# Performance work log

Measured on AMD Instinct MI355X. Metric: run time of the kernel, lower is better.

Reference implementation:

```python
import jax, jax.numpy as jnp
import numpy as np

N_RULES = 64  # R
OUT_PER_RULE = 64  # O, fc out = R*O = 4096


def setup_inputs() -> dict:
    key = jax.random.key(0)
    k1, k2, k3, k4 = jax.random.split(key, 4)
    S, D_IN = 8192, 1024
    RO = N_RULES * OUT_PER_RULE
    X = jax.random.normal(k1, (S, D_IN), dtype=jnp.float32)
    # torch.nn.Linear-style weight [out, in] and bias [out]
    W = jax.random.normal(k2, (RO, D_IN), dtype=jnp.float32) * (1.0 / np.sqrt(D_IN))
    b = jax.random.normal(k3, (RO,), dtype=jnp.float32) * 0.01
    # rule firing strengths (computed under no_grad in the original)
    lambdas = jax.random.uniform(k4, (S, N_RULES), dtype=jnp.float32)
    return {"X": X, "W": W, "b": b, "lambdas": lambdas}


def reference(X, W, b, lambdas):
    # fc + sigmoid: [S, R*O]
    H = jax.nn.sigmoid(X @ W.T + b)
    S = H.shape[0]
    # apply_rule_strength: block-diagonal lambda_eye @ H^T is exactly a
    # rule-weighted sum over the R consecutive O-sized blocks of H.
    Hr = H.reshape(S, N_RULES, OUT_PER_RULE)  # [S, R, O]
    Y = jnp.einsum("sr,sro->so", lambdas, Hr)  # [S, O]
    return Y
```

## Files before the change

kernel.cpp:

```cpp
#include <hip/hip_runtime.h>

#define S_DIM 8192
#define K_DIM 1024
#define RO_DIM 4096
#define O_DIM 64
#define SO (S_DIM * O_DIM)

typedef __attribute__((ext_vector_type(8))) __bf16 bf16x8;
typedef __attribute__((ext_vector_type(4))) float floatx4;
typedef __attribute__((ext_vector_type(4))) unsigned short ushx4;

__device__ inline unsigned short f2bf(float f) {
  unsigned u = __builtin_bit_cast(unsigned, f);
  u += 0x7fff + ((u >> 16) & 1);
  return (unsigned short)(u >> 16);
}
__device__ inline float bf2f(unsigned short h) {
  unsigned u = ((unsigned)h) << 16;
  return __builtin_bit_cast(float, u);
}

__global__ __launch_bounds__(256) void cast_kernel(const float* __restrict__ X,
                                                   const float* __restrict__ W,
                                                   unsigned short* __restrict__ Xb,
                                                   unsigned short* __restrict__ Wb) {
  int i = blockIdx.x * 256 + threadIdx.x;
  const int NX4 = (S_DIM * K_DIM) / 4;
  float4 v;
  unsigned short* dst;
  if (i < NX4) {
    v = ((const float4*)X)[i];
    dst = Xb + (size_t)i * 4;
  } else {
    int j = i - NX4;
    v = ((const float4*)W)[j];
    dst = Wb + (size_t)j * 4;
  }
  ushx4 o;
  o.x = f2bf(v.x); o.y = f2bf(v.y); o.z = f2bf(v.z); o.w = f2bf(v.w);
  *(ushx4*)dst = o;
}

__global__ __launch_bounds__(256) void gemm_kernel(const unsigned short* __restrict__ Xb,
                                                   const unsigned short* __restrict__ Wb,
                                                   const float* __restrict__ bias,
                                                   const float* __restrict__ lam,
                                                   unsigned short* __restrict__ partial) {
  __shared__ __align__(16) unsigned char smem[32768];
  unsigned short* Atile = (unsigned short*)smem;
  unsigned short* Btile = (unsigned short*)(smem + 8192);
  float* ypart = (float*)smem;

  const int t = threadIdx.x;
  const int lane = t & 63;
  const int w = t >> 6;
  const int wm = w & 1;
  const int wn = w >> 1;
  const int quad = lane >> 4;
  const int l16 = lane & 15;
  const int gm0 = blockIdx.y * 128;
  const int gn0 = blockIdx.x * 128;

  floatx4 acc[4][4];
#pragma unroll
  for (int mi = 0; mi < 4; ++mi)
#pragma unroll
    for (int ni = 0; ni < 4; ++ni) acc[mi][ni] = (floatx4){0.f, 0.f, 0.f, 0.f};

  for (int k0 = 0; k0 < K_DIM; k0 += 32) {
    __syncthreads();
#pragma unroll
    for (int i = 0; i < 2; ++i) {
      int idx = i * 256 + t;
      int row = idx >> 2;
      int cc = idx & 3;
      int gcc = cc ^ ((row >> 1) & 3);
      const unsigned short* ga = Xb + (size_t)(gm0 + row) * K_DIM + k0 + gcc * 8;
      const unsigned short* gb = Wb + (size_t)(gn0 + row) * K_DIM + k0 + gcc * 8;
      __builtin_amdgcn_global_load_lds(
          (const __attribute__((address_space(1))) void*)ga,
          (__attribute__((address_space(3))) void*)(Atile + idx * 8), 16, 0, 0);
      __builtin_amdgcn_global_load_lds(
          (const __attribute__((address_space(1))) void*)gb,
          (__attribute__((address_space(3))) void*)(Btile + idx * 8), 16, 0, 0);
    }
    __syncthreads();

    bf16x8 af[4], bfr[4];
#pragma unroll
    for (int mi = 0; mi < 4; ++mi) {
      int row = wm * 64 + mi * 16 + l16;
      int cc = quad ^ ((row >> 1) & 3);
      af[mi] = *(const bf16x8*)(Atile + row * 32 + cc * 8);
    }
#pragma unroll
    for (int ni = 0; ni < 4; ++ni) {
      int row = wn * 64 + ni * 16 + l16;
      int cc = quad ^ ((row >> 1) & 3);
      bfr[ni] = *(const bf16x8*)(Btile + row * 32 + cc * 8);
    }
#pragma unroll
    for (int mi = 0; mi < 4; ++mi)
#pragma unroll
      for (int ni = 0; ni < 4; ++ni)
        acc[mi][ni] = __builtin_amdgcn_mfma_f32_16x16x32_bf16(af[mi], bfr[ni], acc[mi][ni], 0, 0, 0);
  }

  const int rule = blockIdx.x * 2 + wn;
  float bv[4];
#pragma unroll
  for (int ni = 0; ni < 4; ++ni) bv[ni] = bias[gn0 + wn * 64 + ni * 16 + l16];

  __syncthreads();
  if (wn == 0) {
#pragma unroll
    for (int mi = 0; mi < 4; ++mi) {
#pragma unroll
      for (int reg = 0; reg < 4; ++reg) {
        int row = wm * 64 + mi * 16 + quad * 4 + reg;
        float lv = lam[(size_t)(gm0 + row) * 64 + rule];
#pragma unroll
        for (int ni = 0; ni < 4; ++ni) {
          float z = acc[mi][ni][reg] + bv[ni];
          float h = 1.f / (1.f + __expf(-z));
          ypart[row * O_DIM + ni * 16 + l16] = lv * h;
        }
      }
    }
  }
  __syncthreads();
  if (wn == 1) {
#pragma unroll
    for (int mi = 0; mi < 4; ++mi) {
#pragma unroll
      for (int reg = 0; reg < 4; ++reg) {
        int row = wm * 64 + mi * 16 + quad * 4 + reg;
        float lv = lam[(size_t)(gm0 + row) * 64 + rule];
#pragma unroll
        for (int ni = 0; ni < 4; ++ni) {
          float z = acc[mi][ni][reg] + bv[ni];
          float h = 1.f / (1.f + __expf(-z));
          ypart[row * O_DIM + ni * 16 + l16] += lv * h;
        }
      }
    }
  }
  __syncthreads();

  unsigned short* pdst = partial + (size_t)blockIdx.x * SO + (size_t)gm0 * O_DIM;
#pragma unroll
  for (int j = 0; j < 8; ++j) {
    int q = j * 256 + t;
    const float* src = ypart + q * 4;
    ushx4 o;
    o.x = f2bf(src[0]); o.y = f2bf(src[1]); o.z = f2bf(src[2]); o.w = f2bf(src[3]);
    ((ushx4*)pdst)[q] = o;
  }
}

__global__ __launch_bounds__(256) void reduce_kernel(const unsigned short* __restrict__ partial,
                                                     float* __restrict__ Y) {
  int i4 = blockIdx.x * 256 + threadIdx.x;
  float s0 = 0.f, s1 = 0.f, s2 = 0.f, s3 = 0.f;
#pragma unroll
  for (int c = 0; c < 32; ++c) {
    ushx4 v = ((const ushx4*)(partial + (size_t)c * SO))[i4];
    s0 += bf2f(v.x); s1 += bf2f(v.y); s2 += bf2f(v.z); s3 += bf2f(v.w);
  }
  ((float4*)Y)[i4] = (float4){s0, s1, s2, s3};
}

extern "C" void kernel_launch(void* const* d_in, const int* in_sizes, int n_in,
                              void* d_out, int out_size, void* d_ws, size_t ws_size,
                              hipStream_t stream) {
  const float* X = (const float*)d_in[0];
  const float* W = (const float*)d_in[1];
  const float* b = (const float*)d_in[2];
  const float* lam = (const float*)d_in[3];
  float* Y = (float*)d_out;

  unsigned short* Xb = (unsigned short*)d_ws;
  unsigned short* Wb = Xb + (size_t)S_DIM * K_DIM;
  unsigned short* partial = Wb + (size_t)RO_DIM * K_DIM;

  int nCast = ((S_DIM + RO_DIM) * K_DIM / 4) / 256;
  cast_kernel<<<nCast, 256, 0, stream>>>(X, W, Xb, Wb);

  dim3 g(RO_DIM / 128, S_DIM / 128);
  gemm_kernel<<<g, 256, 0, stream>>>(Xb, Wb, b, lam, partial);

  reduce_kernel<<<SO / 1024, 256, 0, stream>>>(partial, Y);
}
```

Before: 206.6 us.

## Switch GEMM to 32x32x16 MFMA and fuse rule reduction via LDS atomics

Replaces the 4x4 grid of 16x16x32 bf16 MFMA tiles per wave with a 2x2 grid of 32x32x16 tiles, split into two k-substeps per 32-wide LDS tile. This cuts the number of LDS fragment loads per MFMA and uses the larger-output instruction. It also seeds the accumulators with the bias, preloads the lambda values into shared memory, and merges the two serialized per-wave-column epilogue phases into one pass of LDS atomicAdd after zeroing. The LDS atomics could contend, though only two waves collide on each address.

```diff
diff --git a/kernel.cpp b/kernel.cpp
--- a/kernel.cpp
+++ b/kernel.cpp
@@ -7,7 +7,7 @@
 #define SO (S_DIM * O_DIM)
 
 typedef __attribute__((ext_vector_type(8))) __bf16 bf16x8;
-typedef __attribute__((ext_vector_type(4))) float floatx4;
+typedef __attribute__((ext_vector_type(16))) float floatx16;
 typedef __attribute__((ext_vector_type(4))) unsigned short ushx4;
 
 __device__ inline unsigned short f2bf(float f) {
@@ -46,26 +46,37 @@
                                                    const float* __restrict__ bias,
                                                    const float* __restrict__ lam,
                                                    unsigned short* __restrict__ partial) {
-  __shared__ __align__(16) unsigned char smem[32768];
+  __shared__ __align__(16) unsigned char smem[33792];
   unsigned short* Atile = (unsigned short*)smem;
   unsigned short* Btile = (unsigned short*)(smem + 8192);
   float* ypart = (float*)smem;
+  float* lamsh = (float*)(smem + 32768);
 
   const int t = threadIdx.x;
   const int lane = t & 63;
   const int w = t >> 6;
   const int wm = w & 1;
   const int wn = w >> 1;
-  const int quad = lane >> 4;
-  const int l16 = lane & 15;
+  const int l32 = lane & 31;
+  const int kg = lane >> 5;
   const int gm0 = blockIdx.y * 128;
   const int gn0 = blockIdx.x * 128;
 
-  floatx4 acc[4][4];
+  {
+    int rl = t >> 7, row = t & 127;
+    lamsh[t] = lam[(size_t)(gm0 + row) * 64 + blockIdx.x * 2 + rl];
+  }
+
+  float bv0 = bias[gn0 + wn * 64 + 0 * 32 + l32];
+  float bv1 = bias[gn0 + wn * 64 + 1 * 32 + l32];
+  floatx16 acc[2][2];
 #pragma unroll
-  for (int mi = 0; mi < 4; ++mi)
+  for (int mi = 0; mi < 2; ++mi)
 #pragma unroll
-    for (int ni = 0; ni < 4; ++ni) acc[mi][ni] = (floatx4){0.f, 0.f, 0.f, 0.f};
+    for (int reg = 0; reg < 16; ++reg) {
+      acc[mi][0][reg] = bv0;
+      acc[mi][1][reg] = bv1;
+    }
 
   for (int k0 = 0; k0 < K_DIM; k0 += 32) {
     __syncthreads();
@@ -86,62 +97,46 @@
     }
     __syncthreads();
 
-    bf16x8 af[4], bfr[4];
 #pragma unroll
-    for (int mi = 0; mi < 4; ++mi) {
-      int row = wm * 64 + mi * 16 + l16;
-      int cc = quad ^ ((row >> 1) & 3);
-      af[mi] = *(const bf16x8*)(Atile + row * 32 + cc * 8);
+    for (int s = 0; s < 2; ++s) {
+      bf16x8 af[2], bfr[2];
+#pragma unroll
+      for (int mi = 0; mi < 2; ++mi) {
+        int row = wm * 64 + mi * 32 + l32;
+        int cc = (s * 2 + kg) ^ ((row >> 1) & 3);
+        af[mi] = *(const bf16x8*)(Atile + row * 32 + cc * 8);
+      }
+#pragma unroll
+      for (int ni = 0; ni < 2; ++ni) {
+        int row = wn * 64 + ni * 32 + l32;
+        int cc = (s * 2 + kg) ^ ((row >> 1) & 3);
+        bfr[ni] = *(const bf16x8*)(Btile + row * 32 + cc * 8);
+      }
+#pragma unroll
+      for (int mi = 0; mi < 2; ++mi)
+#pragma unroll
+        for (int ni = 0; ni < 2; ++ni)
+          acc[mi][ni] = __builtin_amdgcn_mfma_f32_32x32x16_bf16(af[mi], bfr[ni], acc[mi][ni], 0, 0, 0);
     }
-#pragma unroll
-    for (int ni = 0; ni < 4; ++ni) {
-      int row = wn * 64 + ni * 16 + l16;
-      int cc = quad ^ ((row >> 1) & 3);
-      bfr[ni] = *(const bf16x8*)(Btile + row * 32 + cc * 8);
-    }
-#pragma unroll
-    for (int mi = 0; mi < 4; ++mi)
-#pragma unroll
-      for (int ni = 0; ni < 4; ++ni)
-        acc[mi][ni] = __builtin_amdgcn_mfma_f32_16x16x32_bf16(af[mi], bfr[ni], acc[mi][ni], 0, 0, 0);
   }
 
-  const int rule = blockIdx.x * 2 + wn;
-  float bv[4];
+  __syncthreads();
 #pragma unroll
-  for (int ni = 0; ni < 4; ++ni) bv[ni] = bias[gn0 + wn * 64 + ni * 16 + l16];
+  for (int j = 0; j < 8; ++j)
+    ((float4*)ypart)[j * 256 + t] = (float4){0.f, 0.f, 0.f, 0.f};
+  __syncthreads();
 
-  __syncthreads();
-  if (wn == 0) {
 #pragma unroll
-    for (int mi = 0; mi < 4; ++mi) {
+  for (int mi = 0; mi < 2; ++mi) {
 #pragma unroll
-      for (int reg = 0; reg < 4; ++reg) {
-        int row = wm * 64 + mi * 16 + quad * 4 + reg;
-        float lv = lam[(size_t)(gm0 + row) * 64 + rule];
+    for (int reg = 0; reg < 16; ++reg) {
+      int row = wm * 64 + mi * 32 + (reg & 3) + 8 * (reg >> 2) + 4 * kg;
+      float lv = lamsh[wn * 128 + row];
 #pragma unroll
-        for (int ni = 0; ni < 4; ++ni) {
-          float z = acc[mi][ni][reg] + bv[ni];
-          float h = 1.f / (1.f + __expf(-z));
-          ypart[row * O_DIM + ni * 16 + l16] = lv * h;
-        }
-      }
-    }
-  }
-  __syncthreads();
-  if (wn == 1) {
-#pragma unroll
-    for (int mi = 0; mi < 4; ++mi) {
-#pragma unroll
-      for (int reg = 0; reg < 4; ++reg) {
-        int row = wm * 64 + mi * 16 + quad * 4 + reg;
-        float lv = lam[(size_t)(gm0 + row) * 64 + rule];
-#pragma unroll
-        for (int ni = 0; ni < 4; ++ni) {
-          float z = acc[mi][ni][reg] + bv[ni];
-          float h = 1.f / (1.f + __expf(-z));
-          ypart[row * O_DIM + ni * 16 + l16] += lv * h;
-        }
+      for (int ni = 0; ni < 2; ++ni) {
+        float z = acc[mi][ni][reg];
+        float h = 1.f / (1.f + __expf(-z));
+        atomicAdd(&ypart[row * O_DIM + ni * 32 + l32], lv * h);
       }
     }
   }
```

Measured after the change: 336.2 us. 62.7% more time.

## Remap warp N-split so each thread combines both rules in registers

Applied to the files above, without the earlier changes.

Changes the wave-to-column mapping so each wave holds the same output columns for both rules of the 128-wide tile. The rule-weighted sum then happens in registers instead of through a shared-memory staging buffer with extra barriers. Bias is folded into the accumulator initialisation, and lambdas are prefetched into a small LDS array before the K loop. This shrinks LDS use, which may raise occupancy. The cost is that output stores become scattered 2-byte writes instead of vectorised 8-byte stores.

```diff
diff --git a/kernel.cpp b/kernel.cpp
--- a/kernel.cpp
+++ b/kernel.cpp
@@ -46,26 +46,36 @@
                                                    const float* __restrict__ bias,
                                                    const float* __restrict__ lam,
                                                    unsigned short* __restrict__ partial) {
-  __shared__ __align__(16) unsigned char smem[32768];
+  __shared__ __align__(16) unsigned char smem[17408];
   unsigned short* Atile = (unsigned short*)smem;
   unsigned short* Btile = (unsigned short*)(smem + 8192);
-  float* ypart = (float*)smem;
+  float* lamsh = (float*)(smem + 16384);
 
   const int t = threadIdx.x;
   const int lane = t & 63;
   const int w = t >> 6;
   const int wm = w & 1;
-  const int wn = w >> 1;
+  const int oh = w >> 1;
   const int quad = lane >> 4;
   const int l16 = lane & 15;
   const int gm0 = blockIdx.y * 128;
   const int gn0 = blockIdx.x * 128;
 
-  floatx4 acc[4][4];
+  {
+    int row = t >> 1, rl = t & 1;
+    lamsh[t] = lam[(size_t)(gm0 + row) * 64 + blockIdx.x * 2 + rl];
+  }
+
+  floatx4 acc[4][2][2];
 #pragma unroll
-  for (int mi = 0; mi < 4; ++mi)
+  for (int rh = 0; rh < 2; ++rh)
 #pragma unroll
-    for (int ni = 0; ni < 4; ++ni) acc[mi][ni] = (floatx4){0.f, 0.f, 0.f, 0.f};
+    for (int ni = 0; ni < 2; ++ni) {
+      float bv = bias[gn0 + rh * 64 + oh * 32 + ni * 16 + l16];
+#pragma unroll
+      for (int mi = 0; mi < 4; ++mi)
+        acc[mi][rh][ni] = (floatx4){bv, bv, bv, bv};
+    }
 
   for (int k0 = 0; k0 < K_DIM; k0 += 32) {
     __syncthreads();
@@ -86,7 +96,7 @@
     }
     __syncthreads();
 
-    bf16x8 af[4], bfr[4];
+    bf16x8 af[4], bfr[2][2];
 #pragma unroll
     for (int mi = 0; mi < 4; ++mi) {
       int row = wm * 64 + mi * 16 + l16;
@@ -94,67 +104,38 @@
       af[mi] = *(const bf16x8*)(Atile + row * 32 + cc * 8);
     }
 #pragma unroll
-    for (int ni = 0; ni < 4; ++ni) {
-      int row = wn * 64 + ni * 16 + l16;
-      int cc = quad ^ ((row >> 1) & 3);
-      bfr[ni] = *(const bf16x8*)(Btile + row * 32 + cc * 8);
-    }
+    for (int rh = 0; rh < 2; ++rh)
+#pragma unroll
+      for (int ni = 0; ni < 2; ++ni) {
+        int row = rh * 64 + oh * 32 + ni * 16 + l16;
+        int cc = quad ^ ((row >> 1) & 3);
+        bfr[rh][ni] = *(const bf16x8*)(Btile + row * 32 + cc * 8);
+      }
 #pragma unroll
     for (int mi = 0; mi < 4; ++mi)
 #pragma unroll
-      for (int ni = 0; ni < 4; ++ni)
-        acc[mi][ni] = __builtin_amdgcn_mfma_f32_16x16x32_bf16(af[mi], bfr[ni], acc[mi][ni], 0, 0, 0);
+      for (int rh = 0; rh < 2; ++rh)
+#pragma unroll
+        for (int ni = 0; ni < 2; ++ni)
+          acc[mi][rh][ni] =
+              __builtin_amdgcn_mfma_f32_16x16x32_bf16(af[mi], bfr[rh][ni], acc[mi][rh][ni], 0, 0, 0);
   }
 
-  const int rule = blockIdx.x * 2 + wn;
-  float bv[4];
+  unsigned short* pbase = partial + (size_t)blockIdx.x * SO + (size_t)gm0 * O_DIM;
 #pragma unroll
-  for (int ni = 0; ni < 4; ++ni) bv[ni] = bias[gn0 + wn * 64 + ni * 16 + l16];
-
-  __syncthreads();
-  if (wn == 0) {
+  for (int mi = 0; mi < 4; ++mi) {
 #pragma unroll
-    for (int mi = 0; mi < 4; ++mi) {
+    for (int reg = 0; reg < 4; ++reg) {
+      int row = wm * 64 + mi * 16 + quad * 4 + reg;
+      float2 lv = *(const float2*)(lamsh + row * 2);
 #pragma unroll
-      for (int reg = 0; reg < 4; ++reg) {
-        int row = wm * 64 + mi * 16 + quad * 4 + reg;
-        float lv = lam[(size_t)(gm0 + row) * 64 + rule];
-#pragma unroll
-        for (int ni = 0; ni < 4; ++ni) {
-          float z = acc[mi][ni][reg] + bv[ni];
-          float h = 1.f / (1.f + __expf(-z));
-          ypart[row * O_DIM + ni * 16 + l16] = lv * h;
-        }
+      for (int ni = 0; ni < 2; ++ni) {
+        float h0 = 1.f / (1.f + __expf(-acc[mi][0][ni][reg]));
+        float h1 = 1.f / (1.f + __expf(-acc[mi][1][ni][reg]));
+        float y = lv.x * h0 + lv.y * h1;
+        pbase[(size_t)row * O_DIM + oh * 32 + ni * 16 + l16] = f2bf(y);
       }
     }
-  }
-  __syncthreads();
-  if (wn == 1) {
-#pragma unroll
-    for (int mi = 0; mi < 4; ++mi) {
-#pragma unroll
-      for (int reg = 0; reg < 4; ++reg) {
-        int row = wm * 64 + mi * 16 + quad * 4 + reg;
-        float lv = lam[(size_t)(gm0 + row) * 64 + rule];
-#pragma unroll
-        for (int ni = 0; ni < 4; ++ni) {
-          float z = acc[mi][ni][reg] + bv[ni];
-          float h = 1.f / (1.f + __expf(-z));
-          ypart[row * O_DIM + ni * 16 + l16] += lv * h;
-        }
-      }
-    }
-  }
-  __syncthreads();
-
-  unsigned short* pdst = partial + (size_t)blockIdx.x * SO + (size_t)gm0 * O_DIM;
-#pragma unroll
-  for (int j = 0; j < 8; ++j) {
-    int q = j * 256 + t;
-    const float* src = ypart + q * 4;
-    ushx4 o;
-    o.x = f2bf(src[0]); o.y = f2bf(src[1]); o.z = f2bf(src[2]); o.w = f2bf(src[3]);
-    ((ushx4*)pdst)[q] = o;
   }
 }
 
```

After: 200.2 us. -3.1%, faster.
